# Kernel optimization log

Measured on AMD Instinct MI355X. Metric: run time of the kernel, lower is better.

Reference implementation:

```python
import jax, jax.numpy as jnp
import numpy as np

B, T, C, H = 2, 2048, 1024, 16
D = C // H  # head dim = 64
EPS = 1e-5


def layernorm(x, g, b):
    mu = jnp.mean(x, axis=-1, keepdims=True)
    var = jnp.var(x, axis=-1, keepdims=True)
    return (x - mu) * jax.lax.rsqrt(var + EPS) * g + b


def setup_inputs() -> dict:
    key = jax.random.key(0)
    ks = jax.random.split(key, 8)
    init_scale = 0.25
    return {
        "x": jax.random.normal(ks[0], (B, T, C), dtype=jnp.float32),
        # weights stored [in, out] (transpose of torch Linear)
        "w_qkv": jax.random.normal(ks[1], (C, 3 * C), dtype=jnp.float32) * init_scale,
        "b_qkv": jnp.zeros((3 * C,), dtype=jnp.float32),
        "w_proj": jax.random.normal(ks[2], (C, C), dtype=jnp.float32) * init_scale,
        "b_proj": jnp.zeros((C,), dtype=jnp.float32),
        "ln1_g": jnp.ones((C,), dtype=jnp.float32),
        "ln1_b": jnp.zeros((C,), dtype=jnp.float32),
        "w_fc": jax.random.normal(ks[3], (C, 4 * C), dtype=jnp.float32) * init_scale,
        "b_fc": jnp.zeros((4 * C,), dtype=jnp.float32),
        "w_out": jax.random.normal(ks[4], (4 * C, C), dtype=jnp.float32) * init_scale,
        "b_out": jnp.zeros((C,), dtype=jnp.float32),
        "ln2_g": jnp.ones((C,), dtype=jnp.float32),
        "ln2_b": jnp.zeros((C,), dtype=jnp.float32),
    }


def reference(x, w_qkv, b_qkv, w_proj, b_proj, ln1_g, ln1_b,
              w_fc, b_fc, w_out, b_out, ln2_g, ln2_b):
    # ---- attention sub-block (pre-LN) ----
    h = layernorm(x, ln1_g, ln1_b)
    qkv = h @ w_qkv + b_qkv                      # [B,T,3C]
    q, k, v = jnp.split(qkv, 3, axis=-1)
    q = q.reshape(B, T, H, D)
    k = k.reshape(B, T, H, D)
    v = v.reshape(B, T, H, D)
    scores = jnp.einsum('bthd,bshd->bhts', q, k) * (1.0 / np.sqrt(D))
    attn = jax.nn.softmax(scores, axis=-1)       # full [B,H,T,T] as in source
    out = jnp.einsum('bhts,bshd->bthd', attn, v).reshape(B, T, C)
    x = x + out @ w_proj + b_proj
    # ---- MLP sub-block (pre-LN) ----
    h = layernorm(x, ln2_g, ln2_b)
    h = jax.nn.gelu(h @ w_fc + b_fc, approximate=False)  # torch nn.GELU default = exact
    x = x + h @ w_out + b_out
    return x
```

## Files before the change

kernel.cpp:

```cpp
#include <hip/hip_runtime.h>
#include <hip/hip_bf16.h>
#include <math.h>

#define DEVINL static __device__ __forceinline__

typedef _Float16 f16x8 __attribute__((ext_vector_type(8)));
typedef _Float16 f16x4 __attribute__((ext_vector_type(4)));
typedef float f32x4 __attribute__((ext_vector_type(4)));
typedef float f32x16 __attribute__((ext_vector_type(16)));

constexpr int TT = 2048, CC = 1024, HH = 16, DD = 64;
constexpr int HALF_Y = 2 * TT * CC;
constexpr int HALF_L = 2 * HH * TT;

DEVINL void gload_lds16(const void* g, void* s) {
  __builtin_amdgcn_global_load_lds(
      (const __attribute__((address_space(1))) void*)g,
      (__attribute__((address_space(3))) void*)s, 16, 0, 0);
}

DEVINL unsigned pkrtz(float a, float b) {
  typedef __fp16 hf2 __attribute__((ext_vector_type(2)));
  union { hf2 h; unsigned u; } c;
  c.h = __builtin_amdgcn_cvt_pkrtz(a, b);
  return c.u;
}

DEVINL float fast_gelu(float v) {
  float z = v * (2.302208214f + 0.102945116f * v * v);
  return v * __builtin_amdgcn_rcpf(1.0f + exp2f(-z));
}

DEVINL int xcd_swizzle(int lid, int n) {
  int cpx = n >> 3;
  return (lid & 7) * cpx + (lid >> 3);
}

DEVINL void transpose_tile(const float* in, _Float16* out, int K, int N,
                           int bx, int by, int tid) {
  __shared__ float tile[32][33];
  int n0 = bx * 32, k0 = by * 32;
  int tx = tid & 31, ty = tid >> 5;
  #pragma unroll
  for (int i = 0; i < 32; i += 8)
    tile[ty + i][tx] = in[(size_t)(k0 + ty + i) * N + n0 + tx];
  __syncthreads();
  #pragma unroll
  for (int i = 0; i < 32; i += 8)
    out[(size_t)(n0 + ty + i) * K + k0 + tx] = (_Float16)tile[tx][ty + i];
}

DEVINL void ln_row(const float* x, const float* g, const float* bta,
                   _Float16* out, int row, int t) {
  float4 v = ((const float4*)(x + (size_t)row * CC))[t];
  float s = v.x + v.y + v.z + v.w;
  float s2 = v.x * v.x + v.y * v.y + v.z * v.z + v.w * v.w;
  #pragma unroll
  for (int o = 32; o >= 1; o >>= 1) { s += __shfl_xor(s, o); s2 += __shfl_xor(s2, o); }
  __shared__ float ss[4], ssq[4];
  int w = t >> 6;
  if ((t & 63) == 0) { ss[w] = s; ssq[w] = s2; }
  __syncthreads();
  s = ss[0] + ss[1] + ss[2] + ss[3];
  s2 = ssq[0] + ssq[1] + ssq[2] + ssq[3];
  float mu = s * (1.0f / CC);
  float rs = rsqrtf(s2 * (1.0f / CC) - mu * mu + 1e-5f);
  float4 gv = ((const float4*)g)[t];
  float4 bv = ((const float4*)bta)[t];
  f16x4 o4;
  o4[0] = (_Float16)((v.x - mu) * rs * gv.x + bv.x);
  o4[1] = (_Float16)((v.y - mu) * rs * gv.y + bv.y);
  o4[2] = (_Float16)((v.z - mu) * rs * gv.z + bv.z);
  o4[3] = (_Float16)((v.w - mu) * rs * gv.w + bv.w);
  ((f16x4*)(out + (size_t)row * CC))[t] = o4;
}

__global__ __launch_bounds__(256) void prep_all(
    const float* __restrict__ w_qkv, const float* __restrict__ w_proj,
    const float* __restrict__ w_fc, const float* __restrict__ w_out,
    const float* __restrict__ x, const float* __restrict__ ln1_g,
    const float* __restrict__ ln1_b,
    _Float16* __restrict__ wqkv_t, _Float16* __restrict__ wproj_t,
    _Float16* __restrict__ wfc_t, _Float16* __restrict__ wout_t,
    _Float16* __restrict__ h1) {
  int lid = blockIdx.x, t = threadIdx.x;
  if (lid < 3072) {
    transpose_tile(w_qkv, wqkv_t, 1024, 3072, lid % 96, lid / 96, t);
  } else if (lid < 4096) {
    int l = lid - 3072;
    transpose_tile(w_proj, wproj_t, 1024, 1024, l % 32, l / 32, t);
  } else if (lid < 8192) {
    int l = lid - 4096;
    transpose_tile(w_fc, wfc_t, 1024, 4096, l % 128, l / 128, t);
  } else if (lid < 12288) {
    int l = lid - 8192;
    transpose_tile(w_out, wout_t, 4096, 1024, l % 32, l / 32, t);
  } else {
    ln_row(x, ln1_g, ln1_b, h1, lid - 12288, t);
  }
}

__global__ __launch_bounds__(256) void ln_cast(
    const float* __restrict__ x, const float* __restrict__ g,
    const float* __restrict__ bta, _Float16* __restrict__ out) {
  ln_row(x, g, bta, out, blockIdx.x, threadIdx.x);
}

template <int EPI, int N, int K, int BN, int DBUF>
__global__ __launch_bounds__(256) void gemm_bt(
    const _Float16* __restrict__ A, const _Float16* __restrict__ Bt,
    const float* __restrict__ bias, const float* __restrict__ res,
    void* __restrict__ outp, int nbx) {
  constexpr int NWN = BN / 64;
  constexpr int MI = 2 * NWN;
  constexpr int NB = DBUF ? 2 : 1;
  constexpr int NLOADS = 4 + BN / 32;
  __shared__ __align__(16) _Float16 As[NB][128 * 64];
  __shared__ __align__(16) _Float16 Bs[NB][BN * 64];
  const int swz = xcd_swizzle(blockIdx.x, gridDim.x);
  const int bm0 = (swz / nbx) * 128, bn0 = (swz % nbx) * BN;
  const int t = threadIdx.x, w = t >> 6, l = t & 63, lg = l >> 4, lr = l & 15;
  const int wr = w / NWN, wc = w % NWN;
  const int srow = t >> 3, sc = t & 7;
  f32x4 acc[MI][4] = {};

  auto STAGE = [&](int bi, int k0) {
    #pragma unroll
    for (int q = 0; q < 4; ++q) {
      int row = q * 32 + srow;
      int gc = sc ^ (row & 7);
      gload_lds16(A + (size_t)(bm0 + row) * K + k0 + gc * 8, As[bi] + row * 64 + sc * 8);
    }
    #pragma unroll
    for (int q = 0; q < BN / 32; ++q) {
      int row = q * 32 + srow;
      int gc = sc ^ (row & 7);
      gload_lds16(Bt + (size_t)(bn0 + row) * K + k0 + gc * 8, Bs[bi] + row * 64 + sc * 8);
    }
  };
  auto COMPUTE = [&](const _Float16* Ac, const _Float16* Bc) {
    #pragma unroll
    for (int ks = 0; ks < 2; ++ks) {
      f16x8 af[MI], bfr[4];
      #pragma unroll
      for (int mi = 0; mi < MI; ++mi) {
        int row = wr * (16 * MI) + mi * 16 + lr;
        af[mi] = *(const f16x8*)(Ac + row * 64 + (((ks * 4 + lg) ^ (row & 7)) << 3));
      }
      #pragma unroll
      for (int ni = 0; ni < 4; ++ni) {
        int row = wc * 64 + ni * 16 + lr;
        bfr[ni] = *(const f16x8*)(Bc + row * 64 + (((ks * 4 + lg) ^ (row & 7)) << 3));
      }
      #pragma unroll
      for (int mi = 0; mi < MI; ++mi)
        #pragma unroll
        for (int ni = 0; ni < 4; ++ni)
          acc[mi][ni] = __builtin_amdgcn_mfma_f32_16x16x32_f16(af[mi], bfr[ni], acc[mi][ni], 0, 0, 0);
    }
  };

  if constexpr (DBUF) {
    STAGE(0, 0);
    int cur = 0;
    for (int k0 = 0; k0 < K; k0 += 64) {
      if (k0 + 64 < K) {
        STAGE(cur ^ 1, k0 + 64);
        asm volatile("s_waitcnt vmcnt(%0)" :: "i"(NLOADS) : "memory");
      } else {
        asm volatile("s_waitcnt vmcnt(0)" ::: "memory");
      }
      __builtin_amdgcn_s_barrier();
      COMPUTE(As[cur], Bs[cur]);
      __builtin_amdgcn_s_barrier();
      cur ^= 1;
    }
  } else {
    for (int k0 = 0; k0 < K; k0 += 64) {
      STAGE(0, k0);
      __syncthreads();
      COMPUTE(As[0], Bs[0]);
      __syncthreads();
    }
  }

  #pragma unroll
  for (int mi = 0; mi < MI; ++mi) {
    #pragma unroll
    for (int ni = 0; ni < 4; ++ni) {
      int gc = bn0 + wc * 64 + ni * 16 + lr;
      float bv = bias[gc];
      #pragma unroll
      for (int r = 0; r < 4; ++r) {
        int gr = bm0 + wr * (16 * MI) + mi * 16 + lg * 4 + r;
        float v = acc[mi][ni][r] + bv;
        if constexpr (EPI == 1) {
          ((_Float16*)outp)[(size_t)gr * N + gc] = (_Float16)fast_gelu(v);
        } else {
          ((float*)outp)[(size_t)gr * N + gc] = res[(size_t)gr * N + gc] + v;
        }
      }
    }
  }
}

__global__ __launch_bounds__(256) void gemm_qkv(
    const _Float16* __restrict__ A, const _Float16* __restrict__ Bt,
    const float* __restrict__ bias,
    _Float16* __restrict__ qo, _Float16* __restrict__ ko,
    _Float16* __restrict__ vt) {
  __shared__ __align__(16) _Float16 As[128 * 64];
  __shared__ __align__(16) _Float16 Bs[128 * 64];
  const int swz = xcd_swizzle(blockIdx.x, gridDim.x);
  const int bm0 = (swz / 24) * 128, bn0 = (swz % 24) * 128;
  const int t = threadIdx.x, w = t >> 6, l = t & 63, lg = l >> 4, lr = l & 15;
  const int wr = w >> 1, wc = w & 1;
  const int srow = t >> 3, sc = t & 7;
  f32x4 acc[4][4] = {};
  for (int k0 = 0; k0 < 1024; k0 += 64) {
    #pragma unroll
    for (int q = 0; q < 4; ++q) {
      int row = q * 32 + srow;
      int gc = sc ^ (row & 7);
      gload_lds16(A + (size_t)(bm0 + row) * 1024 + k0 + gc * 8, As + row * 64 + sc * 8);
      gload_lds16(Bt + (size_t)(bn0 + row) * 1024 + k0 + gc * 8, Bs + row * 64 + sc * 8);
    }
    __syncthreads();
    #pragma unroll
    for (int ks = 0; ks < 2; ++ks) {
      f16x8 af[4], bfr[4];
      #pragma unroll
      for (int mi = 0; mi < 4; ++mi) {
        int row = wr * 64 + mi * 16 + lr;
        af[mi] = *(const f16x8*)(As + row * 64 + (((ks * 4 + lg) ^ (row & 7)) << 3));
      }
      #pragma unroll
      for (int ni = 0; ni < 4; ++ni) {
        int row = wc * 64 + ni * 16 + lr;
        bfr[ni] = *(const f16x8*)(Bs + row * 64 + (((ks * 4 + lg) ^ (row & 7)) << 3));
      }
      #pragma unroll
      for (int mi = 0; mi < 4; ++mi)
        #pragma unroll
        for (int ni = 0; ni < 4; ++ni)
          acc[mi][ni] = __builtin_amdgcn_mfma_f32_16x16x32_f16(af[mi], bfr[ni], acc[mi][ni], 0, 0, 0);
    }
    __syncthreads();
  }
  const float QSCL = 0.125f * 1.44269504f;
  #pragma unroll
  for (int mi = 0; mi < 4; ++mi) {
    #pragma unroll
    for (int ni = 0; ni < 4; ++ni) {
      int gc = bn0 + wc * 64 + ni * 16 + lr;
      float bv = bias[gc];
      int sec = gc >> 10, cc = gc & 1023;
      #pragma unroll
      for (int r = 0; r < 4; ++r) {
        int gr = bm0 + wr * 64 + mi * 16 + lg * 4 + r;
        float v = acc[mi][ni][r] + bv;
        if (sec == 0) {
          qo[(size_t)gr * 1024 + cc] = (_Float16)(v * QSCL);
        } else if (sec == 1) {
          ko[(size_t)gr * 1024 + cc] = (_Float16)v;
        } else {
          int hh = cc >> 6, dd = cc & 63;
          int bb = gr >> 11, tk = gr & (TT - 1);
          vt[(((size_t)bb * HH + hh) * DD + dd) * TT + tk] = (_Float16)v;
        }
      }
    }
  }
}

__global__ __launch_bounds__(256, 4) void flash_attn(
    const _Float16* __restrict__ qg, const _Float16* __restrict__ kg,
    const _Float16* __restrict__ vt, _Float16* __restrict__ yp,
    float* __restrict__ Lp) {
  const int qt0 = blockIdx.x * 128, h = blockIdx.y;
  const int b = blockIdx.z & 1, half = blockIdx.z >> 1;
  const int kvbeg = half * (TT / 2), kvend = kvbeg + TT / 2;
  const int t = threadIdx.x, w = t >> 6, l = t & 63;
  const int l31 = l & 31, hi = l >> 5;
  __shared__ __align__(16) _Float16 Ks[2][64 * 64];
  __shared__ __align__(16) _Float16 VTs[2][64 * 64];
  const int srow = t >> 3, sc = t & 7;
  const int gc0 = sc ^ (srow & 7) ^ ((srow >> 3) & 7);
  const int gc1 = sc ^ (srow & 7) ^ (((srow >> 3) + 4) & 7);
  const _Float16* kg_r = kg + ((size_t)b * TT + srow) * CC + h * DD;
  const _Float16* vt_r = vt + (((size_t)b * HH + h) * DD + srow) * TT;
  const int dst0 = srow * 64 + sc * 8;

  f16x8 qf[4];
  {
    const _Float16* qp = qg + ((size_t)(b * TT + qt0 + w * 32 + l31)) * CC + h * DD + hi * 8;
    #pragma unroll
    for (int ks = 0; ks < 4; ++ks) qf[ks] = *(const f16x8*)(qp + ks * 16);
  }
  const int rx = l31 & 7, ry = (l31 >> 3) & 7;
  int swk[2], swv[2];
  #pragma unroll
  for (int sub = 0; sub < 2; ++sub) swk[sub] = rx ^ ((sub * 4 + ry) & 7);
  swv[0] = rx ^ ry;
  swv[1] = rx ^ ((4 + ry) & 7);

  f32x16 o0 = {}, o1 = {};
  float osum = 0.0f, mrow = -3.0e38f;

  auto STAGE = [&](int bufi, int kv0) {
    gload_lds16(kg_r + (size_t)kv0 * CC + gc0 * 8, Ks[bufi] + dst0);
    gload_lds16(kg_r + (size_t)(kv0 + 32) * CC + gc1 * 8, Ks[bufi] + 2048 + dst0);
    gload_lds16(vt_r + kv0 + gc0 * 8, VTs[bufi] + dst0);
    gload_lds16(vt_r + 32 * TT + kv0 + gc1 * 8, VTs[bufi] + 2048 + dst0);
  };
  STAGE(0, kvbeg);
  __syncthreads();
  int cur = 0;
  for (int kv0 = kvbeg; kv0 < kvend; kv0 += 64) {
    if (kv0 + 64 < kvend) STAGE(cur ^ 1, kv0 + 64);
    const _Float16* Kc = Ks[cur];
    const _Float16* Vc = VTs[cur];
    #pragma unroll
    for (int sub = 0; sub < 2; ++sub) {
      f32x16 s = {};
      const int krow = (sub * 32 + l31) * 64;
      __builtin_amdgcn_s_setprio(1);
      #pragma unroll
      for (int ks = 0; ks < 4; ++ks) {
        f16x8 kf = *(const f16x8*)(Kc + krow + (((ks * 2 + hi) ^ swk[sub]) << 3));
        s = __builtin_amdgcn_mfma_f32_32x32x16_f16(kf, qf[ks], s, 0, 0, 0);
      }
      __builtin_amdgcn_s_setprio(0);
      float m01 = fmaxf(fmaxf(s[0], s[1]), fmaxf(s[2], s[3]));
      float m23 = fmaxf(fmaxf(s[4], s[5]), fmaxf(s[6], s[7]));
      float m45 = fmaxf(fmaxf(s[8], s[9]), fmaxf(s[10], s[11]));
      float m67 = fmaxf(fmaxf(s[12], s[13]), fmaxf(s[14], s[15]));
      float m16v = fmaxf(fmaxf(m01, m23), fmaxf(m45, m67));
      int ok = (m16v <= mrow + 8.0f) ? 1 : 0;
      if (!__all(ok)) {
        float mo = fmaxf(m16v, __shfl_xor(m16v, 32));
        float mn = fmaxf(mrow, mo);
        float corr = exp2f(mrow - mn);
        mrow = mn;
        #pragma unroll
        for (int r = 0; r < 16; ++r) { o0[r] *= corr; o1[r] *= corr; }
        osum *= corr;
      }
      float p[16];
      float psum = 0.0f;
      #pragma unroll
      for (int r = 0; r < 16; ++r) { p[r] = exp2f(s[r] - mrow); psum += p[r]; }
      osum += psum;
      unsigned W[8], X[8];
      #pragma unroll
      for (int i = 0; i < 8; ++i) {
        W[i] = pkrtz(p[2 * i], p[2 * i + 1]);
        X[i] = __shfl_xor(W[i], 32);
      }
      union { unsigned u[4]; f16x8 v; } bp[2];
      #pragma unroll
      for (int s2 = 0; s2 < 2; ++s2) {
        bp[s2].u[0] = hi ? X[4 * s2 + 2] : W[4 * s2 + 0];
        bp[s2].u[1] = hi ? X[4 * s2 + 3] : W[4 * s2 + 1];
        bp[s2].u[2] = hi ? W[4 * s2 + 2] : X[4 * s2 + 0];
        bp[s2].u[3] = hi ? W[4 * s2 + 3] : X[4 * s2 + 1];
      }
      __builtin_amdgcn_s_setprio(1);
      #pragma unroll
      for (int s2 = 0; s2 < 2; ++s2) {
        int c = sub * 4 + s2 * 2 + hi;
        {
          f16x8 vf = *(const f16x8*)(Vc + l31 * 64 + ((c ^ swv[0]) << 3));
          o0 = __builtin_amdgcn_mfma_f32_32x32x16_f16(vf, bp[s2].v, o0, 0, 0, 0);
        }
        {
          f16x8 vf = *(const f16x8*)(Vc + (32 + l31) * 64 + ((c ^ swv[1]) << 3));
          o1 = __builtin_amdgcn_mfma_f32_32x32x16_f16(vf, bp[s2].v, o1, 0, 0, 0);
        }
      }
      __builtin_amdgcn_s_setprio(0);
    }
    __syncthreads();
    cur ^= 1;
  }
  osum += __shfl_xor(osum, 32);
  float rinv = 1.0f / osum;
  const int qrow = qt0 + w * 32 + l31;
  _Float16* ob = yp + (size_t)half * HALF_Y + ((size_t)(b * TT + qrow)) * CC + h * DD;
  #pragma unroll
  for (int i = 0; i < 4; ++i) {
    int col0 = 8 * i + 4 * hi;
    uint2 v0, v1;
    v0.x = pkrtz(o0[4 * i + 0] * rinv, o0[4 * i + 1] * rinv);
    v0.y = pkrtz(o0[4 * i + 2] * rinv, o0[4 * i + 3] * rinv);
    v1.x = pkrtz(o1[4 * i + 0] * rinv, o1[4 * i + 1] * rinv);
    v1.y = pkrtz(o1[4 * i + 2] * rinv, o1[4 * i + 3] * rinv);
    *(uint2*)(ob + col0) = v0;
    *(uint2*)(ob + 32 + col0) = v1;
  }
  if (hi == 0)
    Lp[(size_t)half * HALF_L + ((size_t)b * HH + h) * TT + qrow] =
        mrow + log2f(osum);
}

__global__ __launch_bounds__(256) void attn_combine(
    const _Float16* __restrict__ yp, const float* __restrict__ Lp,
    _Float16* __restrict__ att) {
  int bt = blockIdx.x;
  int b = bt >> 11, tt = bt & (TT - 1);
  int tid = threadIdx.x;
  int h = tid >> 4;
  size_t li = ((size_t)b * HH + h) * TT + tt;
  float L0 = Lp[li], L1 = Lp[HALF_L + li];
  float m = fmaxf(L0, L1);
  float w0 = exp2f(L0 - m), w1 = exp2f(L1 - m);
  float rs = 1.0f / (w0 + w1);
  w0 *= rs; w1 *= rs;
  f16x4 a = ((const f16x4*)(yp + (size_t)bt * CC))[tid];
  f16x4 c = ((const f16x4*)(yp + HALF_Y + (size_t)bt * CC))[tid];
  f16x4 o;
  #pragma unroll
  for (int i = 0; i < 4; ++i)
    o[i] = (_Float16)(w0 * (float)a[i] + w1 * (float)c[i]);
  ((f16x4*)(att + (size_t)bt * CC))[tid] = o;
}

extern "C" void kernel_launch(void* const* d_in, const int* in_sizes, int n_in,
                              void* d_out, int out_size, void* d_ws, size_t ws_size,
                              hipStream_t stream) {
  const float* x      = (const float*)d_in[0];
  const float* w_qkv  = (const float*)d_in[1];
  const float* b_qkv  = (const float*)d_in[2];
  const float* w_proj = (const float*)d_in[3];
  const float* b_proj = (const float*)d_in[4];
  const float* ln1_g  = (const float*)d_in[5];
  const float* ln1_b  = (const float*)d_in[6];
  const float* w_fc   = (const float*)d_in[7];
  const float* b_fc   = (const float*)d_in[8];
  const float* w_out  = (const float*)d_in[9];
  const float* b_out  = (const float*)d_in[10];
  const float* ln2_g  = (const float*)d_in[11];
  const float* ln2_b  = (const float*)d_in[12];

  char* ws = (char*)d_ws;
  _Float16* wqkv_t = (_Float16*)(ws);
  _Float16* wproj_t= (_Float16*)(ws + 6291456);
  _Float16* wfc_t  = (_Float16*)(ws + 8388608);
  _Float16* wout_t = (_Float16*)(ws + 16777216);
  _Float16* hslot  = (_Float16*)(ws + 25165824);
  _Float16* qbuf   = (_Float16*)(ws + 33554432);
  _Float16* kbuf   = (_Float16*)(ws + 41943040);
  _Float16* vtbuf  = (_Float16*)(ws + 50331648);
  _Float16* tbuf   = (_Float16*)(ws + 33554432);
  float*    x1     = (float*)(ws + 67108864);
  _Float16* ypart  = (_Float16*)(ws + 83886080);
  float*    Lpart  = (float*)(ws + 100663296);

  prep_all<<<16384, 256, 0, stream>>>(w_qkv, w_proj, w_fc, w_out, x, ln1_g, ln1_b,
                                      wqkv_t, wproj_t, wfc_t, wout_t, hslot);
  gemm_qkv<<<768, 256, 0, stream>>>(hslot, wqkv_t, b_qkv, qbuf, kbuf, vtbuf);
  flash_attn<<<dim3(16, 16, 4), 256, 0, stream>>>(qbuf, kbuf, vtbuf, ypart, Lpart);
  attn_combine<<<4096, 256, 0, stream>>>(ypart, Lpart, hslot);
  gemm_bt<2, 1024, 1024, 64, 1><<<512, 256, 0, stream>>>(hslot, wproj_t, b_proj, x, x1, 16);
  ln_cast<<<4096, 256, 0, stream>>>(x1, ln2_g, ln2_b, hslot);
  gemm_bt<1, 4096, 1024, 128, 0><<<1024, 256, 0, stream>>>(hslot, wfc_t, b_fc, nullptr, tbuf, 32);
  gemm_bt<2, 1024, 4096, 64, 1><<<512, 256, 0, stream>>>(tbuf, wout_t, b_out, x1, (float*)d_out, 16);
}
```

Baseline: 279.3 us.

## Double-buffer all GEMMs with BK=32 tiles and compute softmax row sums via MFMA

All GEMMs (qkv, fc, proj, out) now use a double-buffered K loop with 32-wide K tiles and a new 4-chunk XOR swizzle, so the global-to-LDS loads of the next tile overlap the current tile's MFMAs. The previously single-buffered qkv and fc GEMMs gain this overlap, while LDS per block stays about the same. In flash attention, the per-row softmax sum is now accumulated by an extra MFMA against a ones vector instead of scalar adds plus a cross-lane shuffle, and the max reduction tree is reshaped. The trade-offs are twice as many barriers per K, one extra MFMA per PV step, and halved per-barrier work.

Measured after the change: 292.5 us. 4.7% more time.

```diff
diff --git a/kernel.cpp b/kernel.cpp
--- a/kernel.cpp
+++ b/kernel.cpp
@@ -106,82 +106,70 @@
   ln_row(x, g, bta, out, blockIdx.x, threadIdx.x);
 }
 
-template <int EPI, int N, int K, int BN, int DBUF>
+template <int EPI, int N, int K, int BN>
 __global__ __launch_bounds__(256) void gemm_bt(
     const _Float16* __restrict__ A, const _Float16* __restrict__ Bt,
     const float* __restrict__ bias, const float* __restrict__ res,
     void* __restrict__ outp, int nbx) {
   constexpr int NWN = BN / 64;
   constexpr int MI = 2 * NWN;
-  constexpr int NB = DBUF ? 2 : 1;
-  constexpr int NLOADS = 4 + BN / 32;
-  __shared__ __align__(16) _Float16 As[NB][128 * 64];
-  __shared__ __align__(16) _Float16 Bs[NB][BN * 64];
+  constexpr int NLOADS = 2 + BN / 64;
+  __shared__ __align__(16) _Float16 As[2][128 * 32];
+  __shared__ __align__(16) _Float16 Bs[2][BN * 32];
   const int swz = xcd_swizzle(blockIdx.x, gridDim.x);
   const int bm0 = (swz / nbx) * 128, bn0 = (swz % nbx) * BN;
   const int t = threadIdx.x, w = t >> 6, l = t & 63, lg = l >> 4, lr = l & 15;
   const int wr = w / NWN, wc = w % NWN;
-  const int srow = t >> 3, sc = t & 7;
+  const int srow4 = t >> 2;
+  const int gch = (t & 3) ^ ((t >> 3) & 3);
   f32x4 acc[MI][4] = {};
 
   auto STAGE = [&](int bi, int k0) {
     #pragma unroll
-    for (int q = 0; q < 4; ++q) {
-      int row = q * 32 + srow;
-      int gc = sc ^ (row & 7);
-      gload_lds16(A + (size_t)(bm0 + row) * K + k0 + gc * 8, As[bi] + row * 64 + sc * 8);
-    }
-    #pragma unroll
-    for (int q = 0; q < BN / 32; ++q) {
-      int row = q * 32 + srow;
-      int gc = sc ^ (row & 7);
-      gload_lds16(Bt + (size_t)(bn0 + row) * K + k0 + gc * 8, Bs[bi] + row * 64 + sc * 8);
+    for (int q = 0; q < 2; ++q) {
+      int row = q * 64 + srow4;
+      gload_lds16(A + (size_t)(bm0 + row) * K + k0 + gch * 8,
+                  As[bi] + q * 2048 + t * 8);
+    }
+    #pragma unroll
+    for (int q = 0; q < BN / 64; ++q) {
+      int row = q * 64 + srow4;
+      gload_lds16(Bt + (size_t)(bn0 + row) * K + k0 + gch * 8,
+                  Bs[bi] + q * 2048 + t * 8);
     }
   };
   auto COMPUTE = [&](const _Float16* Ac, const _Float16* Bc) {
-    #pragma unroll
-    for (int ks = 0; ks < 2; ++ks) {
-      f16x8 af[MI], bfr[4];
-      #pragma unroll
-      for (int mi = 0; mi < MI; ++mi) {
-        int row = wr * (16 * MI) + mi * 16 + lr;
-        af[mi] = *(const f16x8*)(Ac + row * 64 + (((ks * 4 + lg) ^ (row & 7)) << 3));
-      }
-      #pragma unroll
-      for (int ni = 0; ni < 4; ++ni) {
-        int row = wc * 64 + ni * 16 + lr;
-        bfr[ni] = *(const f16x8*)(Bc + row * 64 + (((ks * 4 + lg) ^ (row & 7)) << 3));
-      }
-      #pragma unroll
-      for (int mi = 0; mi < MI; ++mi)
-        #pragma unroll
-        for (int ni = 0; ni < 4; ++ni)
-          acc[mi][ni] = __builtin_amdgcn_mfma_f32_16x16x32_f16(af[mi], bfr[ni], acc[mi][ni], 0, 0, 0);
-    }
+    f16x8 af[MI], bfr[4];
+    #pragma unroll
+    for (int mi = 0; mi < MI; ++mi) {
+      int row = wr * (16 * MI) + mi * 16 + lr;
+      af[mi] = *(const f16x8*)(Ac + row * 32 + ((lg ^ ((row >> 1) & 3)) << 3));
+    }
+    #pragma unroll
+    for (int ni = 0; ni < 4; ++ni) {
+      int row = wc * 64 + ni * 16 + lr;
+      bfr[ni] = *(const f16x8*)(Bc + row * 32 + ((lg ^ ((row >> 1) & 3)) << 3));
+    }
+    #pragma unroll
+    for (int mi = 0; mi < MI; ++mi)
+      #pragma unroll
+      for (int ni = 0; ni < 4; ++ni)
+        acc[mi][ni] = __builtin_amdgcn_mfma_f32_16x16x32_f16(af[mi], bfr[ni], acc[mi][ni], 0, 0, 0);
   };
 
-  if constexpr (DBUF) {
-    STAGE(0, 0);
-    int cur = 0;
-    for (int k0 = 0; k0 < K; k0 += 64) {
-      if (k0 + 64 < K) {
-        STAGE(cur ^ 1, k0 + 64);
-        asm volatile("s_waitcnt vmcnt(%0)" :: "i"(NLOADS) : "memory");
-      } else {
-        asm volatile("s_waitcnt vmcnt(0)" ::: "memory");
-      }
-      __builtin_amdgcn_s_barrier();
-      COMPUTE(As[cur], Bs[cur]);
-      __builtin_amdgcn_s_barrier();
-      cur ^= 1;
-    }
-  } else {
-    for (int k0 = 0; k0 < K; k0 += 64) {
-      STAGE(0, k0);
-      __syncthreads();
-      COMPUTE(As[0], Bs[0]);
-      __syncthreads();
-    }
+  STAGE(0, 0);
+  int cur = 0;
+  for (int k0 = 0; k0 < K; k0 += 32) {
+    if (k0 + 32 < K) {
+      STAGE(cur ^ 1, k0 + 32);
+      asm volatile("s_waitcnt vmcnt(%0)" :: "i"(NLOADS) : "memory");
+    } else {
+      asm volatile("s_waitcnt vmcnt(0)" ::: "memory");
+    }
+    __builtin_amdgcn_s_barrier();
+    COMPUTE(As[cur], Bs[cur]);
+    __builtin_amdgcn_s_barrier();
+    cur ^= 1;
   }
 
   #pragma unroll
@@ -209,44 +197,60 @@
     const float* __restrict__ bias,
     _Float16* __restrict__ qo, _Float16* __restrict__ ko,
     _Float16* __restrict__ vt) {
-  __shared__ __align__(16) _Float16 As[128 * 64];
-  __shared__ __align__(16) _Float16 Bs[128 * 64];
+  __shared__ __align__(16) _Float16 As[2][128 * 32];
+  __shared__ __align__(16) _Float16 Bs[2][128 * 32];
   const int swz = xcd_swizzle(blockIdx.x, gridDim.x);
   const int bm0 = (swz / 24) * 128, bn0 = (swz % 24) * 128;
   const int t = threadIdx.x, w = t >> 6, l = t & 63, lg = l >> 4, lr = l & 15;
   const int wr = w >> 1, wc = w & 1;
-  const int srow = t >> 3, sc = t & 7;
+  const int srow4 = t >> 2;
+  const int gch = (t & 3) ^ ((t >> 3) & 3);
   f32x4 acc[4][4] = {};
-  for (int k0 = 0; k0 < 1024; k0 += 64) {
-    #pragma unroll
-    for (int q = 0; q < 4; ++q) {
-      int row = q * 32 + srow;
-      int gc = sc ^ (row & 7);
-      gload_lds16(A + (size_t)(bm0 + row) * 1024 + k0 + gc * 8, As + row * 64 + sc * 8);
-      gload_lds16(Bt + (size_t)(bn0 + row) * 1024 + k0 + gc * 8, Bs + row * 64 + sc * 8);
-    }
-    __syncthreads();
-    #pragma unroll
-    for (int ks = 0; ks < 2; ++ks) {
-      f16x8 af[4], bfr[4];
-      #pragma unroll
-      for (int mi = 0; mi < 4; ++mi) {
-        int row = wr * 64 + mi * 16 + lr;
-        af[mi] = *(const f16x8*)(As + row * 64 + (((ks * 4 + lg) ^ (row & 7)) << 3));
-      }
-      #pragma unroll
-      for (int ni = 0; ni < 4; ++ni) {
-        int row = wc * 64 + ni * 16 + lr;
-        bfr[ni] = *(const f16x8*)(Bs + row * 64 + (((ks * 4 + lg) ^ (row & 7)) << 3));
-      }
-      #pragma unroll
-      for (int mi = 0; mi < 4; ++mi)
-        #pragma unroll
-        for (int ni = 0; ni < 4; ++ni)
-          acc[mi][ni] = __builtin_amdgcn_mfma_f32_16x16x32_f16(af[mi], bfr[ni], acc[mi][ni], 0, 0, 0);
-    }
-    __syncthreads();
-  }
+
+  auto STAGE = [&](int bi, int k0) {
+    #pragma unroll
+    for (int q = 0; q < 2; ++q) {
+      int row = q * 64 + srow4;
+      gload_lds16(A + (size_t)(bm0 + row) * 1024 + k0 + gch * 8,
+                  As[bi] + q * 2048 + t * 8);
+      gload_lds16(Bt + (size_t)(bn0 + row) * 1024 + k0 + gch * 8,
+                  Bs[bi] + q * 2048 + t * 8);
+    }
+  };
+  auto COMPUTE = [&](const _Float16* Ac, const _Float16* Bc) {
+    f16x8 af[4], bfr[4];
+    #pragma unroll
+    for (int mi = 0; mi < 4; ++mi) {
+      int row = wr * 64 + mi * 16 + lr;
+      af[mi] = *(const f16x8*)(Ac + row * 32 + ((lg ^ ((row >> 1) & 3)) << 3));
+    }
+    #pragma unroll
+    for (int ni = 0; ni < 4; ++ni) {
+      int row = wc * 64 + ni * 16 + lr;
+      bfr[ni] = *(const f16x8*)(Bc + row * 32 + ((lg ^ ((row >> 1) & 3)) << 3));
+    }
+    #pragma unroll
+    for (int mi = 0; mi < 4; ++mi)
+      #pragma unroll
+      for (int ni = 0; ni < 4; ++ni)
+        acc[mi][ni] = __builtin_amdgcn_mfma_f32_16x16x32_f16(af[mi], bfr[ni], acc[mi][ni], 0, 0, 0);
+  };
+
+  STAGE(0, 0);
+  int cur = 0;
+  for (int k0 = 0; k0 < 1024; k0 += 32) {
+    if (k0 + 32 < 1024) {
+      STAGE(cur ^ 1, k0 + 32);
+      asm volatile("s_waitcnt vmcnt(4)" ::: "memory");
+    } else {
+      asm volatile("s_waitcnt vmcnt(0)" ::: "memory");
+    }
+    __builtin_amdgcn_s_barrier();
+    COMPUTE(As[cur], Bs[cur]);
+    __builtin_amdgcn_s_barrier();
+    cur ^= 1;
+  }
+
   const float QSCL = 0.125f * 1.44269504f;
   #pragma unroll
   for (int mi = 0; mi < 4; ++mi) {
@@ -305,7 +309,10 @@
   swv[1] = rx ^ ((4 + ry) & 7);
 
   f32x16 o0 = {}, o1 = {};
-  float osum = 0.0f, mrow = -3.0e38f;
+  f32x16 osacc = {};
+  float mrow = -3.0e38f;
+  const f16x8 onesA = {(_Float16)1, (_Float16)1, (_Float16)1, (_Float16)1,
+                       (_Float16)1, (_Float16)1, (_Float16)1, (_Float16)1};
 
   auto STAGE = [&](int bufi, int kv0) {
     gload_lds16(kg_r + (size_t)kv0 * CC + gc0 * 8, Ks[bufi] + dst0);
@@ -331,11 +338,12 @@
         s = __builtin_amdgcn_mfma_f32_32x32x16_f16(kf, qf[ks], s, 0, 0, 0);
       }
       __builtin_amdgcn_s_setprio(0);
-      float m01 = fmaxf(fmaxf(s[0], s[1]), fmaxf(s[2], s[3]));
-      float m23 = fmaxf(fmaxf(s[4], s[5]), fmaxf(s[6], s[7]));
-      float m45 = fmaxf(fmaxf(s[8], s[9]), fmaxf(s[10], s[11]));
-      float m67 = fmaxf(fmaxf(s[12], s[13]), fmaxf(s[14], s[15]));
-      float m16v = fmaxf(fmaxf(m01, m23), fmaxf(m45, m67));
+      float a0 = fmaxf(fmaxf(s[0], s[1]), s[2]);
+      float a1 = fmaxf(fmaxf(s[3], s[4]), s[5]);
+      float a2 = fmaxf(fmaxf(s[6], s[7]), s[8]);
+      float a3 = fmaxf(fmaxf(s[9], s[10]), s[11]);
+      float a4 = fmaxf(fmaxf(s[12], s[13]), s[14]);
+      float m16v = fmaxf(fmaxf(fmaxf(a0, a1), a2), fmaxf(fmaxf(a3, a4), s[15]));
       int ok = (m16v <= mrow + 8.0f) ? 1 : 0;
       if (!__all(ok)) {
         float mo = fmaxf(m16v, __shfl_xor(m16v, 32));
@@ -344,13 +352,11 @@
         mrow = mn;
         #pragma unroll
         for (int r = 0; r < 16; ++r) { o0[r] *= corr; o1[r] *= corr; }
-        osum *= corr;
+        osacc[0] *= corr;
       }
       float p[16];
-      float psum = 0.0f;
-      #pragma unroll
-      for (int r = 0; r < 16; ++r) { p[r] = exp2f(s[r] - mrow); psum += p[r]; }
-      osum += psum;
+      #pragma unroll
+      for (int r = 0; r < 16; ++r) p[r] = exp2f(s[r] - mrow);
       unsigned W[8], X[8];
       #pragma unroll
       for (int i = 0; i < 8; ++i) {
@@ -377,13 +383,14 @@
           f16x8 vf = *(const f16x8*)(Vc + (32 + l31) * 64 + ((c ^ swv[1]) << 3));
           o1 = __builtin_amdgcn_mfma_f32_32x32x16_f16(vf, bp[s2].v, o1, 0, 0, 0);
         }
+        osacc = __builtin_amdgcn_mfma_f32_32x32x16_f16(onesA, bp[s2].v, osacc, 0, 0, 0);
       }
       __builtin_amdgcn_s_setprio(0);
     }
     __syncthreads();
     cur ^= 1;
   }
-  osum += __shfl_xor(osum, 32);
+  float osum = osacc[0];
   float rinv = 1.0f / osum;
   const int qrow = qt0 + w * 32 + l31;
   _Float16* ob = yp + (size_t)half * HALF_Y + ((size_t)(b * TT + qrow)) * CC + h * DD;
@@ -461,8 +468,8 @@
   gemm_qkv<<<768, 256, 0, stream>>>(hslot, wqkv_t, b_qkv, qbuf, kbuf, vtbuf);
   flash_attn<<<dim3(16, 16, 4), 256, 0, stream>>>(qbuf, kbuf, vtbuf, ypart, Lpart);
   attn_combine<<<4096, 256, 0, stream>>>(ypart, Lpart, hslot);
-  gemm_bt<2, 1024, 1024, 64, 1><<<512, 256, 0, stream>>>(hslot, wproj_t, b_proj, x, x1, 16);
+  gemm_bt<2, 1024, 1024, 64><<<512, 256, 0, stream>>>(hslot, wproj_t, b_proj, x, x1, 16);
   ln_cast<<<4096, 256, 0, stream>>>(x1, ln2_g, ln2_b, hslot);
-  gemm_bt<1, 4096, 1024, 128, 0><<<1024, 256, 0, stream>>>(hslot, wfc_t, b_fc, nullptr, tbuf, 32);
-  gemm_bt<2, 1024, 4096, 64, 1><<<512, 256, 0, stream>>>(tbuf, wout_t, b_out, x1, (float*)d_out, 16);
-}
+  gemm_bt<1, 4096, 1024, 128><<<1024, 256, 0, stream>>>(hslot, wfc_t, b_fc, nullptr, tbuf, 32);
+  gemm_bt<2, 1024, 4096, 64><<<512, 256, 0, stream>>>(tbuf, wout_t, b_out, x1, (float*)d_out, 16);
+}
```
